# Kernel tuning notes

Measured on AMD Instinct MI355X. Metric: run time of the kernel, lower is better.

The kernel has to match this reference:

```python
import jax, jax.numpy as jnp
import numpy as np

N, NC, G, C = 80000, 8000, 16, 5
E, ES = 160000, 80000
NUM_OPS, OP_E, OP_F, CFG_F, H = 120, 32, 140, 18, 32
ALPHA = 0.2  # tf.nn.leaky_relu default slope

seg = jax.ops.segment_sum

def lrelu(x):
    return jnp.where(x >= 0, x, ALPHA * x)

def l2norm(x):
    s = jnp.sum(x * x, axis=-1, keepdims=True)
    return x * jax.lax.rsqrt(jnp.maximum(s, 1e-12))

def setup_inputs():
    k = jax.random.split(jax.random.key(0), 20)
    p = lambda i, shp, s=0.1: jax.random.normal(k[i], shp, jnp.float32) * s
    d_in = CFG_F + OP_F + OP_E  # 190: concat(config, op feats, op embed)
    d_gc = CFG_F + H            # 50: concat(config, hidden)
    return {
        'op_feats': jax.random.normal(k[0], (N, OP_F), jnp.float32),
        'config_feats': jax.random.normal(k[1], (NC, C, CFG_F), jnp.float32),
        'op_ids': jax.random.randint(k[2], (N,), 0, NUM_OPS),
        'selected': jax.random.randint(k[3], (N,), 0, 2) == 1,
        'feed_src': jax.random.randint(k[4], (E,), 0, N),
        'feed_dst': jax.random.randint(k[5], (E,), 0, N),
        'sfeed_src': jax.random.randint(k[6], (ES,), 0, N),
        'sfeed_dst': jax.random.randint(k[7], (ES,), 0, N),
        'config_src': jnp.arange(NC),
        'config_dst': jax.random.randint(k[8], (NC,), 0, N),
        'sconfig_src': jnp.arange(NC),
        'sconfig_dst': jax.random.randint(k[9], (NC,), 0, N),
        'op_gid': (jnp.arange(N) * G) // N,
        'cfg_gid': (jnp.arange(NC) * G) // NC,
        'emb': p(10, (NUM_OPS, OP_E), 1.0),
        'pre_w1': p(11, (d_in, H)), 'pre_b1': jnp.zeros((H,), jnp.float32),
        'pre_w2': p(12, (H, H)), 'pre_b2': jnp.zeros((H,), jnp.float32),
        'gc1_w1': p(13, (d_gc, H)), 'gc1_b1': jnp.zeros((H,), jnp.float32),
        'gc1_w2': p(14, (H, H)), 'gc1_b2': jnp.zeros((H,), jnp.float32),
        'gc2_w1': p(15, (d_gc, H)), 'gc2_b1': jnp.zeros((H,), jnp.float32),
        'gc2_w2': p(16, (H, H)), 'gc2_b2': jnp.zeros((H,), jnp.float32),
        'post_w1': p(17, (3 * H, H)),
        'post_w2': p(18, (H, 1)),
    }

def _mlp(x, w1, b1, w2, b2):
    return lrelu(x @ w1 + b1) @ w2 + b2

def _node_forward(nf, cf, src, dst, csrc, cdst, pre, gcs):
    # AdjacencyMultiplier('config') @ config_feats : scatter nconfig feats to ops
    cfg = 100.0 * seg(cf[csrc], cdst, num_segments=N)            # [N, C, 18]
    x = jnp.broadcast_to(nf[:, None, :], (N, C, nf.shape[-1]))   # stack over configs
    x = lrelu(_mlp(jnp.concatenate([cfg, x], -1), *pre))         # prenet + leaky_relu
    # A_hat = A + A^T + I with symmetric normalization D^-1/2 A_hat D^-1/2
    loop = jnp.arange(N)
    src_all = jnp.concatenate([src, dst, loop])
    dst_all = jnp.concatenate([dst, src, loop])
    inv = jax.lax.rsqrt(seg(jnp.ones(src_all.shape, nf.dtype), dst_all, num_segments=N))
    inv = inv[:, None, None]
    for gp in gcs:
        y = jnp.concatenate([cfg, x], -1) * inv
        y = seg(y[src_all], dst_all, num_segments=N) * inv       # A_hat_norm @ y
        x = x + lrelu(_mlp(y, *gp))                              # residual
    return x

def _forward(op_feats, config_feats, emb, pre, gc1, gc2, post_w1, post_w2,
             op_ids, selected, feed, sfeed, cfg_e, scfg_e, op_gid, cfg_gid):
    nf = jnp.concatenate([op_feats, emb[op_ids]], -1)            # [N, 172]
    x_full = _node_forward(jax.lax.stop_gradient(nf), jax.lax.stop_gradient(config_feats),
                           feed[0], feed[1], cfg_e[0], cfg_e[1], pre, (gc1, gc2))
    x_bp = _node_forward(nf, config_feats, sfeed[0], sfeed[1],
                         scfg_e[0], scfg_e[1], pre, (gc1, gc2))
    x = jnp.where(selected[:, None, None], x_bp, x_full)         # [N, C, H]
    cfg_nodes = seg(x[cfg_e[1]], cfg_e[0], num_segments=NC)      # adj_config^T @ x
    op_sum = seg(x, op_gid, num_segments=G)                      # [G, C, H]
    cnt = seg(jnp.ones((N,), x.dtype), op_gid, num_segments=G)
    op_mean = op_sum / cnt[:, None, None]
    cfg_sum = seg(cfg_nodes, cfg_gid, num_segments=G)
    feats = jnp.concatenate([op_mean, l2norm(op_sum), l2norm(cfg_sum)], -1)  # [G, C, 3H]
    return (lrelu(feats @ post_w1) @ post_w2)[..., 0]            # [G, C]

def reference(op_feats, config_feats, op_ids, selected, feed_src, feed_dst,
              sfeed_src, sfeed_dst, config_src, config_dst, sconfig_src, sconfig_dst,
              op_gid, cfg_gid, emb, pre_w1, pre_b1, pre_w2, pre_b2,
              gc1_w1, gc1_b1, gc1_w2, gc1_b2, gc2_w1, gc2_b1, gc2_w2, gc2_b2,
              post_w1, post_w2):
    return _forward(op_feats, config_feats, emb,
                    (pre_w1, pre_b1, pre_w2, pre_b2),
                    (gc1_w1, gc1_b1, gc1_w2, gc1_b2),
                    (gc2_w1, gc2_b1, gc2_w2, gc2_b2),
                    post_w1, post_w2,
                    op_ids, selected, (feed_src, feed_dst), (sfeed_src, sfeed_dst),
                    (config_src, config_dst), (sconfig_src, sconfig_dst), op_gid, cfg_gid)
```

## Files before the change

### kernel.cpp

```cpp
#include <hip/hip_runtime.h>
#include <hip/hip_bf16.h>
#include <math.h>

#define CDIV(a,b) (((a)+(b)-1)/(b))

constexpr int N_   = 80000;
constexpr int NC_  = 8000;
constexpr int G_   = 16;
constexpr int C_   = 5;
constexpr int CFGF = 18;
constexpr int OPF  = 140;
constexpr int OPE  = 32;
constexpr int H_   = 32;
constexpr int NUMOPS = 120;
constexpr int CROW = C_ * CFGF;
constexpr int XROW = C_ * H_;
constexpr float ALPHA_ = 0.2f;
constexpr int NPG = N_ / G_;
constexpr int EPG = NC_ / G_;

__device__ __forceinline__ float lrelu(float v) { return v >= 0.0f ? v : ALPHA_ * v; }

__global__ void k_nfwop(const float* __restrict__ emb, const float* __restrict__ w1,
                        const float* __restrict__ b1, float* __restrict__ nfwop) {
    int t = blockIdx.x * blockDim.x + threadIdx.x;
    if (t >= NUMOPS * H_) return;
    int op = t >> 5, h = t & 31;
    float a = b1[h];
    for (int e = 0; e < OPE; ++e)
        a = fmaf(emb[op * OPE + e], w1[(CFGF + OPF + e) * H_ + h], a);
    nfwop[t] = a;
}

__global__ void k_nfw(const float* __restrict__ opf, const int* __restrict__ op_ids,
                      const float* __restrict__ nfwop, const float* __restrict__ w1,
                      float* __restrict__ nfw) {
    int n = blockIdx.x * blockDim.x + threadIdx.x;
    if (n >= N_) return;
    float acc[H_];
    const float4* it = (const float4*)(nfwop + (size_t)op_ids[n] * H_);
    #pragma unroll
    for (int q = 0; q < 8; ++q) {
        float4 v = it[q];
        acc[4 * q + 0] = v.x; acc[4 * q + 1] = v.y; acc[4 * q + 2] = v.z; acc[4 * q + 3] = v.w;
    }
    const float4* f4 = (const float4*)(opf + (size_t)n * OPF);
    const float* wf = w1 + CFGF * H_;
    for (int kc = 0; kc < OPF / 4; ++kc) {
        float4 rv = f4[kc];
        float rs[4] = {rv.x, rv.y, rv.z, rv.w};
        #pragma unroll
        for (int j = 0; j < 4; ++j) {
            int k = kc * 4 + j;
            #pragma unroll
            for (int h = 0; h < H_; ++h) acc[h] = fmaf(rs[j], wf[k * H_ + h], acc[h]);
        }
    }
    float4* o = (float4*)(nfw + (size_t)n * H_);
    #pragma unroll
    for (int q = 0; q < 8; ++q)
        o[q] = make_float4(acc[4 * q], acc[4 * q + 1], acc[4 * q + 2], acc[4 * q + 3]);
}

__global__ void k_cfg_scatter(const float* __restrict__ cf, const int* __restrict__ cdst,
                              float* __restrict__ cfg) {
    int t = blockIdx.x * blockDim.x + threadIdx.x;
    if (t >= NC_ * CROW) return;
    int i = t / CROW, j = t - i * CROW;
    atomicAdd(&cfg[(size_t)cdst[i] * CROW + j], 100.0f * cf[t]);
}

__global__ void k_deg2(const int* __restrict__ s0, const int* __restrict__ d0, int E0,
                       const int* __restrict__ s1, const int* __restrict__ d1, int E1,
                       int* __restrict__ deg) {
    int e = blockIdx.x * blockDim.x + threadIdx.x;
    if (e < E0) {
        atomicAdd(&deg[s0[e]], 1);
        atomicAdd(&deg[d0[e]], 1);
    } else if (e < E0 + E1) {
        int e2 = e - E0;
        atomicAdd(&deg[N_ + s1[e2]], 1);
        atomicAdd(&deg[N_ + d1[e2]], 1);
    }
}

__global__ void k_inv2(const int* __restrict__ deg, float* __restrict__ inv) {
    int i = blockIdx.x * blockDim.x + threadIdx.x;
    if (i >= 2 * N_) return;
    inv[i] = 1.0f / sqrtf((float)(deg[i] + 1));
}

__global__ void k_scan1(const int* __restrict__ deg, int* __restrict__ roff, int* __restrict__ aux) {
    __shared__ int s[256];
    int t = threadIdx.x, n = blockIdx.x * 256 + t;
    int v = (n < 2 * N_) ? deg[n] : 0;
    s[t] = v; __syncthreads();
    for (int off = 1; off < 256; off <<= 1) {
        int x = (t >= off) ? s[t - off] : 0;
        __syncthreads();
        s[t] += x;
        __syncthreads();
    }
    if (n < 2 * N_) roff[n] = s[t] - v;
    if (t == 255) aux[blockIdx.x] = s[255];
}

__global__ void k_scan2(int* __restrict__ aux, int nb) {
    __shared__ int s[1024];
    int t = threadIdx.x;
    int v = (t < nb) ? aux[t] : 0;
    s[t] = v; __syncthreads();
    for (int off = 1; off < 1024; off <<= 1) {
        int x = (t >= off) ? s[t - off] : 0;
        __syncthreads();
        s[t] += x;
        __syncthreads();
    }
    if (t < nb) aux[t] = s[t] - v;
}

__global__ void k_scan3(int* __restrict__ roff, const int* __restrict__ aux,
                        int* __restrict__ cur, int total) {
    int n = blockIdx.x * blockDim.x + threadIdx.x;
    if (n < 2 * N_) {
        int r = roff[n] + aux[n >> 8];
        roff[n] = r;
        cur[n] = r;
    }
    if (n == 0) roff[2 * N_] = total;
}

__global__ void k_fill2(const int* __restrict__ s0, const int* __restrict__ d0, int E0,
                        const int* __restrict__ s1, const int* __restrict__ d1, int E1,
                        int* __restrict__ cur, int* __restrict__ col) {
    int e = blockIdx.x * blockDim.x + threadIdx.x;
    if (e < E0) {
        int s = s0[e], d = d0[e];
        col[atomicAdd(&cur[d], 1)] = s;
        col[atomicAdd(&cur[s], 1)] = d;
    } else if (e < E0 + E1) {
        int e2 = e - E0;
        int s = s1[e2], d = d1[e2];
        col[atomicAdd(&cur[N_ + d], 1)] = s;
        col[atomicAdd(&cur[N_ + s], 1)] = d;
    }
}

__global__ void k_csum_gather(const float2* __restrict__ cfg2, const float* __restrict__ inv,
                              const int* __restrict__ roff, const int* __restrict__ col,
                              float2* __restrict__ csum2) {
    int t = blockIdx.x * blockDim.x + threadIdx.x;
    if (t >= N_ * 45) return;
    int n = t / 45, j2 = t - n * 45;
    float iv = inv[n];
    float2 a = cfg2[t];
    a.x *= iv; a.y *= iv;
    int e = roff[n], p1 = roff[n + 1];
    for (; e + 1 < p1; e += 2) {
        int s0 = col[e], s1 = col[e + 1];
        float i0 = inv[s0], i1 = inv[s1];
        float2 v0 = cfg2[(size_t)s0 * 45 + j2];
        float2 v1 = cfg2[(size_t)s1 * 45 + j2];
        a.x = fmaf(v0.x, i0, a.x); a.y = fmaf(v0.y, i0, a.y);
        a.x = fmaf(v1.x, i1, a.x); a.y = fmaf(v1.y, i1, a.y);
    }
    if (e < p1) {
        int s0 = col[e];
        float i0 = inv[s0];
        float2 v0 = cfg2[(size_t)s0 * 45 + j2];
        a.x = fmaf(v0.x, i0, a.x); a.y = fmaf(v0.y, i0, a.y);
    }
    csum2[t] = a;
}

__global__ void k_pre(const float* __restrict__ cfg, const float* __restrict__ nfw,
                      const float* __restrict__ w1, const float* __restrict__ w2,
                      const float* __restrict__ b2, float* __restrict__ x) {
    int r = blockIdx.x * blockDim.x + threadIdx.x;
    if (r >= N_ * C_) return;
    int n = r / C_;
    float h1[H_];
    const float4* nf4 = (const float4*)(nfw + (size_t)n * H_);
    #pragma unroll
    for (int q = 0; q < 8; ++q) {
        float4 v = nf4[q];
        h1[4 * q + 0] = v.x; h1[4 * q + 1] = v.y; h1[4 * q + 2] = v.z; h1[4 * q + 3] = v.w;
    }
    const float2* c2 = (const float2*)(cfg + (size_t)r * CFGF);
    for (int kc = 0; kc < CFGF / 2; ++kc) {
        float2 cv = c2[kc];
        float cs[2] = {cv.x, cv.y};
        #pragma unroll
        for (int j = 0; j < 2; ++j) {
            int k = kc * 2 + j;
            #pragma unroll
            for (int h = 0; h < H_; ++h) h1[h] = fmaf(cs[j], w1[k * H_ + h], h1[h]);
        }
    }
    #pragma unroll
    for (int h = 0; h < H_; ++h) h1[h] = lrelu(h1[h]);
    float acc[H_];
    #pragma unroll
    for (int h = 0; h < H_; ++h) acc[h] = b2[h];
    #pragma unroll
    for (int k = 0; k < H_; ++k) {
        float v = h1[k];
        #pragma unroll
        for (int h = 0; h < H_; ++h) acc[h] = fmaf(v, w2[k * H_ + h], acc[h]);
    }
    float4* o = (float4*)(x + (size_t)r * H_);
    #pragma unroll
    for (int q = 0; q < 8; ++q)
        o[q] = make_float4(lrelu(acc[4 * q]), lrelu(acc[4 * q + 1]),
                           lrelu(acc[4 * q + 2]), lrelu(acc[4 * q + 3]));
}

__global__ void k_gcfused(const float4* __restrict__ xin4, const float* __restrict__ csum,
                          const float* __restrict__ inv, const int* __restrict__ roff,
                          const int* __restrict__ col,
                          const float* __restrict__ w1, const float* __restrict__ b1,
                          const float* __restrict__ w2, const float* __restrict__ b2,
                          float4* __restrict__ xout4) {
    int r = blockIdx.x * blockDim.x + threadIdx.x;
    if (r >= N_ * C_) return;
    int n = r / C_, c = r - n * C_;
    float iv = inv[n];
    float xs[H_];
    const float4* sp = xin4 + (size_t)r * 8;
    #pragma unroll
    for (int q = 0; q < 8; ++q) {
        float4 v = sp[q];
        xs[4 * q + 0] = v.x * iv; xs[4 * q + 1] = v.y * iv;
        xs[4 * q + 2] = v.z * iv; xs[4 * q + 3] = v.w * iv;
    }
    int e = roff[n], p1 = roff[n + 1];
    for (; e + 1 < p1; e += 2) {
        int s0 = col[e], s1 = col[e + 1];
        float i0 = inv[s0], i1 = inv[s1];
        const float4* np0 = xin4 + ((size_t)s0 * C_ + c) * 8;
        const float4* np1 = xin4 + ((size_t)s1 * C_ + c) * 8;
        #pragma unroll
        for (int q = 0; q < 8; ++q) {
            float4 v0 = np0[q];
            float4 v1 = np1[q];
            xs[4 * q + 0] = fmaf(v0.x, i0, xs[4 * q + 0]);
            xs[4 * q + 1] = fmaf(v0.y, i0, xs[4 * q + 1]);
            xs[4 * q + 2] = fmaf(v0.z, i0, xs[4 * q + 2]);
            xs[4 * q + 3] = fmaf(v0.w, i0, xs[4 * q + 3]);
            xs[4 * q + 0] = fmaf(v1.x, i1, xs[4 * q + 0]);
            xs[4 * q + 1] = fmaf(v1.y, i1, xs[4 * q + 1]);
            xs[4 * q + 2] = fmaf(v1.z, i1, xs[4 * q + 2]);
            xs[4 * q + 3] = fmaf(v1.w, i1, xs[4 * q + 3]);
        }
    }
    if (e < p1) {
        int s0 = col[e];
        float i0 = inv[s0];
        const float4* np = xin4 + ((size_t)s0 * C_ + c) * 8;
        #pragma unroll
        for (int q = 0; q < 8; ++q) {
            float4 v = np[q];
            xs[4 * q + 0] = fmaf(v.x, i0, xs[4 * q + 0]);
            xs[4 * q + 1] = fmaf(v.y, i0, xs[4 * q + 1]);
            xs[4 * q + 2] = fmaf(v.z, i0, xs[4 * q + 2]);
            xs[4 * q + 3] = fmaf(v.w, i0, xs[4 * q + 3]);
        }
    }
    float t1[H_];
    #pragma unroll
    for (int h = 0; h < H_; ++h) t1[h] = 0.0f;
    const float2* c2 = (const float2*)(csum + (size_t)r * CFGF);
    for (int kc = 0; kc < CFGF / 2; ++kc) {
        float2 cv = c2[kc];
        float cs[2] = {cv.x, cv.y};
        #pragma unroll
        for (int j = 0; j < 2; ++j) {
            int k = kc * 2 + j;
            #pragma unroll
            for (int h = 0; h < H_; ++h) t1[h] = fmaf(cs[j], w1[k * H_ + h], t1[h]);
        }
    }
    #pragma unroll
    for (int k = 0; k < H_; ++k) {
        float v = xs[k];
        #pragma unroll
        for (int h = 0; h < H_; ++h) t1[h] = fmaf(v, w1[(CFGF + k) * H_ + h], t1[h]);
    }
    float h1[H_];
    #pragma unroll
    for (int h = 0; h < H_; ++h) h1[h] = lrelu(fmaf(iv, t1[h], b1[h]));
    float acc[H_];
    #pragma unroll
    for (int h = 0; h < H_; ++h) acc[h] = b2[h];
    #pragma unroll
    for (int k = 0; k < H_; ++k) {
        float v = h1[k];
        #pragma unroll
        for (int h = 0; h < H_; ++h) acc[h] = fmaf(v, w2[k * H_ + h], acc[h]);
    }
    float4* o = xout4 + (size_t)r * 8;
    #pragma unroll
    for (int q = 0; q < 8; ++q) {
        float4 v = sp[q];
        v.x += lrelu(acc[4 * q + 0]); v.y += lrelu(acc[4 * q + 1]);
        v.z += lrelu(acc[4 * q + 2]); v.w += lrelu(acc[4 * q + 3]);
        o[q] = v;
    }
}

__global__ void k_opsum(const float4* __restrict__ xf4, const float4* __restrict__ xb4,
                        const int* __restrict__ sel,
                        float* __restrict__ osum, float* __restrict__ cnt) {
    __shared__ float4 ls[6 * G_ * 40];
    __shared__ float lc[6 * G_];
    for (int i = threadIdx.x; i < 6 * G_ * 40; i += blockDim.x) ls[i] = make_float4(0.f, 0.f, 0.f, 0.f);
    if (threadIdx.x < 6 * G_) lc[threadIdx.x] = 0.0f;
    __syncthreads();
    int j4 = threadIdx.x % 40, i = threadIdx.x / 40;
    const int NPB = CDIV(N_, 512);
    int start = blockIdx.x * NPB;
    int end = min(start + NPB, N_);
    if (i < 6) {
        for (int n = start + i; n < end; n += 6) {
            int g = n / NPG;
            const float4* xr = sel[n] ? xb4 : xf4;
            float4 v = xr[(size_t)n * 40 + j4];
            int o = (i * G_ + g) * 40 + j4;
            float4 cacc = ls[o];
            cacc.x += v.x; cacc.y += v.y; cacc.z += v.z; cacc.w += v.w;
            ls[o] = cacc;
            if (j4 == 0) lc[i * G_ + g] += 1.0f;
        }
    }
    __syncthreads();
    for (int idx = threadIdx.x; idx < G_ * 40; idx += blockDim.x) {
        float4 s = ls[idx];
        #pragma unroll
        for (int q = 1; q < 6; ++q) {
            float4 v = ls[q * G_ * 40 + idx];
            s.x += v.x; s.y += v.y; s.z += v.z; s.w += v.w;
        }
        int g = idx / 40, j = idx - g * 40;
        float* o = osum + (size_t)g * XROW + j * 4;
        atomicAdd(o + 0, s.x); atomicAdd(o + 1, s.y);
        atomicAdd(o + 2, s.z); atomicAdd(o + 3, s.w);
    }
    if (threadIdx.x < G_) {
        float c = 0.0f;
        #pragma unroll
        for (int q = 0; q < 6; ++q) c += lc[q * G_ + threadIdx.x];
        atomicAdd(&cnt[threadIdx.x], c);
    }
}

__global__ void k_cfgsum(const float4* __restrict__ xf4, const float4* __restrict__ xb4,
                         const int* __restrict__ sel, const int* __restrict__ cdst,
                         float* __restrict__ gsum) {
    __shared__ float4 ls[6 * G_ * 40];
    for (int i = threadIdx.x; i < 6 * G_ * 40; i += blockDim.x) ls[i] = make_float4(0.f, 0.f, 0.f, 0.f);
    __syncthreads();
    int j4 = threadIdx.x % 40, i = threadIdx.x / 40;
    const int EPB = CDIV(NC_, 64);
    int start = blockIdx.x * EPB;
    int end = min(start + EPB, NC_);
    if (i < 6) {
        for (int e = start + i; e < end; e += 6) {
            int g = e / EPG;
            int n = cdst[e];
            const float4* xr = sel[n] ? xb4 : xf4;
            float4 v = xr[(size_t)n * 40 + j4];
            int o = (i * G_ + g) * 40 + j4;
            float4 cacc = ls[o];
            cacc.x += v.x; cacc.y += v.y; cacc.z += v.z; cacc.w += v.w;
            ls[o] = cacc;
        }
    }
    __syncthreads();
    for (int idx = threadIdx.x; idx < G_ * 40; idx += blockDim.x) {
        float4 s = ls[idx];
        #pragma unroll
        for (int q = 1; q < 6; ++q) {
            float4 v = ls[q * G_ * 40 + idx];
            s.x += v.x; s.y += v.y; s.z += v.z; s.w += v.w;
        }
        int g = idx / 40, j = idx - g * 40;
        float* o = gsum + (size_t)g * XROW + j * 4;
        atomicAdd(o + 0, s.x); atomicAdd(o + 1, s.y);
        atomicAdd(o + 2, s.z); atomicAdd(o + 3, s.w);
    }
}

__global__ void k_final(const float* __restrict__ osum, const float* __restrict__ gsum,
                        const float* __restrict__ cnt, const float* __restrict__ pw1,
                        const float* __restrict__ pw2, float* __restrict__ out) {
    __shared__ float sw1[3 * H_ * H_];
    __shared__ float sw2[H_];
    for (int i = threadIdx.x; i < 3 * H_ * H_; i += blockDim.x) sw1[i] = pw1[i];
    if (threadIdx.x < H_) sw2[threadIdx.x] = pw2[threadIdx.x];
    __syncthreads();
    int t = threadIdx.x;
    if (t >= G_ * C_) return;
    int g = t / C_;
    const float* os = osum + (size_t)t * H_;
    const float* cs = gsum + (size_t)t * H_;
    float icnt = 1.0f / cnt[g];
    float a0[H_], a1[H_], a2[H_];
    float s1 = 0.0f, s2 = 0.0f;
    #pragma unroll
    for (int h = 0; h < H_; ++h) {
        float v1 = os[h], v2 = cs[h];
        a0[h] = v1 * icnt;
        a1[h] = v1; s1 = fmaf(v1, v1, s1);
        a2[h] = v2; s2 = fmaf(v2, v2, s2);
    }
    float r1 = 1.0f / sqrtf(fmaxf(s1, 1e-12f));
    float r2 = 1.0f / sqrtf(fmaxf(s2, 1e-12f));
    #pragma unroll
    for (int h = 0; h < H_; ++h) { a1[h] *= r1; a2[h] *= r2; }
    float o = 0.0f;
    #pragma unroll
    for (int h = 0; h < H_; ++h) {
        float a = 0.0f;
        #pragma unroll
        for (int k = 0; k < H_; ++k) a = fmaf(a0[k], sw1[k * H_ + h], a);
        #pragma unroll
        for (int k = 0; k < H_; ++k) a = fmaf(a1[k], sw1[(H_ + k) * H_ + h], a);
        #pragma unroll
        for (int k = 0; k < H_; ++k) a = fmaf(a2[k], sw1[(2 * H_ + k) * H_ + h], a);
        o = fmaf(lrelu(a), sw2[h], o);
    }
    out[t] = o;
}

extern "C" void kernel_launch(void* const* d_in, const int* in_sizes, int n_in,
                              void* d_out, int out_size, void* d_ws, size_t ws_size,
                              hipStream_t stream) {
    const float* op_feats     = (const float*)d_in[0];
    const float* config_feats = (const float*)d_in[1];
    const int*   op_ids       = (const int*)d_in[2];
    const int*   selected     = (const int*)d_in[3];
    const int*   feed_src     = (const int*)d_in[4];
    const int*   feed_dst     = (const int*)d_in[5];
    const int*   sfeed_src    = (const int*)d_in[6];
    const int*   sfeed_dst    = (const int*)d_in[7];
    const int*   config_dst   = (const int*)d_in[9];
    const int*   sconfig_dst  = (const int*)d_in[11];
    const float* emb          = (const float*)d_in[14];
    const float* pre_w1       = (const float*)d_in[15];
    const float* pre_b1       = (const float*)d_in[16];
    const float* pre_w2       = (const float*)d_in[17];
    const float* pre_b2       = (const float*)d_in[18];
    const float* gc_w1[2]     = {(const float*)d_in[19], (const float*)d_in[23]};
    const float* gc_b1[2]     = {(const float*)d_in[20], (const float*)d_in[24]};
    const float* gc_w2[2]     = {(const float*)d_in[21], (const float*)d_in[25]};
    const float* gc_b2[2]     = {(const float*)d_in[22], (const float*)d_in[26]};
    const float* post_w1      = (const float*)d_in[27];
    const float* post_w2      = (const float*)d_in[28];

    int E0 = in_sizes[4], E1 = in_sizes[6];

    char* ws = (char*)d_ws;
    size_t off = 0;
    auto alloc = [&](size_t bytes) { void* p = ws + off; off += (bytes + 255) & ~(size_t)255; return p; };
    float* nfw   = (float*)alloc((size_t)N_ * H_ * 4);
    float* nfwop = (float*)alloc((size_t)NUMOPS * H_ * 4);
    float* cfg   = (float*)alloc((size_t)N_ * CROW * 4);
    float* csum  = (float*)alloc((size_t)N_ * CROW * 4);
    float* xf    = (float*)alloc((size_t)N_ * XROW * 4);
    float* xb    = (float*)alloc((size_t)N_ * XROW * 4);
    float* xscr  = (float*)alloc((size_t)N_ * XROW * 4);
    float* invA  = (float*)alloc((size_t)2 * N_ * 4);
    int*   degA  = (int*)alloc((size_t)2 * N_ * 4);
    int*   roffA = (int*)alloc((size_t)(2 * N_ + 1) * 4);
    int*   curA  = (int*)alloc((size_t)2 * N_ * 4);
    int*   aux   = (int*)alloc((size_t)1024 * 4);
    int*   colA  = (int*)alloc((size_t)2 * (E0 + E1) * 4);
    float* osum  = (float*)alloc((size_t)G_ * XROW * 4);
    float* gsum  = (float*)alloc((size_t)G_ * XROW * 4);
    float* cntb  = (float*)alloc((size_t)G_ * 4);

    const int NB1 = CDIV(2 * N_, 256);

    k_nfwop<<<CDIV(NUMOPS * H_, 256), 256, 0, stream>>>(emb, pre_w1, pre_b1, nfwop);
    k_nfw<<<CDIV(N_, 256), 256, 0, stream>>>(op_feats, op_ids, nfwop, pre_w1, nfw);

    hipMemsetAsync(degA, 0, (size_t)2 * N_ * 4, stream);
    k_deg2<<<CDIV(E0 + E1, 256), 256, 0, stream>>>(feed_src, feed_dst, E0,
                                                   sfeed_src, sfeed_dst, E1, degA);
    k_inv2<<<CDIV(2 * N_, 256), 256, 0, stream>>>(degA, invA);
    k_scan1<<<NB1, 256, 0, stream>>>(degA, roffA, aux);
    k_scan2<<<1, 1024, 0, stream>>>(aux, NB1);
    k_scan3<<<CDIV(2 * N_, 256), 256, 0, stream>>>(roffA, aux, curA, 2 * (E0 + E1));
    k_fill2<<<CDIV(E0 + E1, 256), 256, 0, stream>>>(feed_src, feed_dst, E0,
                                                    sfeed_src, sfeed_dst, E1, curA, colA);

    for (int p = 0; p < 2; ++p) {
        const int* cdst = p ? sconfig_dst : config_dst;
        float* x0 = p ? xb : xf;
        const float* ivp = invA + (size_t)p * N_;
        const int* roffp = roffA + (size_t)p * N_;

        hipMemsetAsync(cfg, 0, (size_t)N_ * CROW * 4, stream);
        k_cfg_scatter<<<CDIV(NC_ * CROW, 256), 256, 0, stream>>>(config_feats, cdst, cfg);
        k_csum_gather<<<CDIV(N_ * 45, 256), 256, 0, stream>>>((const float2*)cfg, ivp, roffp,
                                                              colA, (float2*)csum);
        k_pre<<<CDIV(N_ * C_, 256), 256, 0, stream>>>(cfg, nfw, pre_w1, pre_w2, pre_b2, x0);

        k_gcfused<<<CDIV(N_ * C_, 256), 256, 0, stream>>>((const float4*)x0, csum, ivp, roffp,
                                                          colA, gc_w1[0], gc_b1[0], gc_w2[0],
                                                          gc_b2[0], (float4*)xscr);
        k_gcfused<<<CDIV(N_ * C_, 256), 256, 0, stream>>>((const float4*)xscr, csum, ivp, roffp,
                                                          colA, gc_w1[1], gc_b1[1], gc_w2[1],
                                                          gc_b2[1], (float4*)x0);
    }

    hipMemsetAsync(osum, 0, (size_t)(2 * G_ * XROW + G_) * 4, stream);
    k_opsum<<<512, 256, 0, stream>>>((const float4*)xf, (const float4*)xb, selected, osum, cntb);
    k_cfgsum<<<64, 256, 0, stream>>>((const float4*)xf, (const float4*)xb, selected,
                                     config_dst, gsum);
    k_final<<<1, 128, 0, stream>>>(osum, gsum, cntb, post_w1, post_w2, (float*)d_out);
}
```

Measured before the change: 715.9 us.

## Sort nodes by degree so gather wavefronts process similar neighbor counts

Adds a per-graph degree histogram, a bucket scan and a counting sort that build a node permutation ordered by descending degree. The neighbor-gather kernels for config sums and graph convolution now map each thread to a permuted node. Threads in a wavefront therefore iterate over similar neighbor counts, which is meant to cut divergence and idle lanes in the edge loops. In exchange it adds three small launches plus atomics, and reads and writes of each node's own row no longer follow thread order, which may hurt coalescing.

```diff
diff --git a/kernel.cpp b/kernel.cpp
--- a/kernel.cpp
+++ b/kernel.cpp
@@ -146,16 +146,45 @@
     }
 }
 
+__global__ void k_hist(const int* __restrict__ deg, int* __restrict__ hist) {
+    int i = blockIdx.x * blockDim.x + threadIdx.x;
+    if (i >= 2 * N_) return;
+    int b = (i >= N_ ? 256 : 0) + min(deg[i], 255);
+    atomicAdd(&hist[b], 1);
+}
+
+__global__ void k_hscan(const int* __restrict__ hist, int* __restrict__ cur) {
+    __shared__ int s[512];
+    int t = threadIdx.x;
+    s[t] = hist[t];
+    __syncthreads();
+    int half = t & 256, d = t & 255;
+    int sum = 0;
+    for (int dd = d + 1; dd < 256; ++dd) sum += s[half + dd];
+    cur[t] = sum;
+}
+
+__global__ void k_psort(const int* __restrict__ deg, int* __restrict__ cur,
+                        int* __restrict__ perm) {
+    int i = blockIdx.x * blockDim.x + threadIdx.x;
+    if (i >= 2 * N_) return;
+    int p = i >= N_;
+    int b = (p ? 256 : 0) + min(deg[i], 255);
+    int pos = atomicAdd(&cur[b], 1);
+    perm[p * N_ + pos] = i - p * N_;
+}
+
 __global__ void k_csum_gather(const float2* __restrict__ cfg2, const float* __restrict__ inv,
                               const int* __restrict__ roff, const int* __restrict__ col,
-                              float2* __restrict__ csum2) {
+                              const int* __restrict__ perm, float2* __restrict__ csum2) {
     int t = blockIdx.x * blockDim.x + threadIdx.x;
     if (t >= N_ * 45) return;
-    int n = t / 45, j2 = t - n * 45;
-    float iv = inv[n];
-    float2 a = cfg2[t];
+    int q = t / 45, j2 = t - q * 45;
+    int nl = perm[q];
+    float iv = inv[nl];
+    float2 a = cfg2[(size_t)nl * 45 + j2];
     a.x *= iv; a.y *= iv;
-    int e = roff[n], p1 = roff[n + 1];
+    int e = roff[nl], p1 = roff[nl + 1];
     for (; e + 1 < p1; e += 2) {
         int s0 = col[e], s1 = col[e + 1];
         float i0 = inv[s0], i1 = inv[s1];
@@ -217,40 +246,41 @@
 
 __global__ void k_gcfused(const float4* __restrict__ xin4, const float* __restrict__ csum,
                           const float* __restrict__ inv, const int* __restrict__ roff,
-                          const int* __restrict__ col,
+                          const int* __restrict__ col, const int* __restrict__ perm,
                           const float* __restrict__ w1, const float* __restrict__ b1,
                           const float* __restrict__ w2, const float* __restrict__ b2,
                           float4* __restrict__ xout4) {
     int r = blockIdx.x * blockDim.x + threadIdx.x;
     if (r >= N_ * C_) return;
-    int n = r / C_, c = r - n * C_;
-    float iv = inv[n];
+    int q = r / C_, c = r - q * C_;
+    int nl = perm[q];
+    float iv = inv[nl];
     float xs[H_];
-    const float4* sp = xin4 + (size_t)r * 8;
-    #pragma unroll
-    for (int q = 0; q < 8; ++q) {
-        float4 v = sp[q];
-        xs[4 * q + 0] = v.x * iv; xs[4 * q + 1] = v.y * iv;
-        xs[4 * q + 2] = v.z * iv; xs[4 * q + 3] = v.w * iv;
-    }
-    int e = roff[n], p1 = roff[n + 1];
+    const float4* sp = xin4 + ((size_t)nl * C_ + c) * 8;
+    #pragma unroll
+    for (int qq = 0; qq < 8; ++qq) {
+        float4 v = sp[qq];
+        xs[4 * qq + 0] = v.x * iv; xs[4 * qq + 1] = v.y * iv;
+        xs[4 * qq + 2] = v.z * iv; xs[4 * qq + 3] = v.w * iv;
+    }
+    int e = roff[nl], p1 = roff[nl + 1];
     for (; e + 1 < p1; e += 2) {
         int s0 = col[e], s1 = col[e + 1];
         float i0 = inv[s0], i1 = inv[s1];
         const float4* np0 = xin4 + ((size_t)s0 * C_ + c) * 8;
         const float4* np1 = xin4 + ((size_t)s1 * C_ + c) * 8;
         #pragma unroll
-        for (int q = 0; q < 8; ++q) {
-            float4 v0 = np0[q];
-            float4 v1 = np1[q];
-            xs[4 * q + 0] = fmaf(v0.x, i0, xs[4 * q + 0]);
-            xs[4 * q + 1] = fmaf(v0.y, i0, xs[4 * q + 1]);
-            xs[4 * q + 2] = fmaf(v0.z, i0, xs[4 * q + 2]);
-            xs[4 * q + 3] = fmaf(v0.w, i0, xs[4 * q + 3]);
-            xs[4 * q + 0] = fmaf(v1.x, i1, xs[4 * q + 0]);
-            xs[4 * q + 1] = fmaf(v1.y, i1, xs[4 * q + 1]);
-            xs[4 * q + 2] = fmaf(v1.z, i1, xs[4 * q + 2]);
-            xs[4 * q + 3] = fmaf(v1.w, i1, xs[4 * q + 3]);
+        for (int qq = 0; qq < 8; ++qq) {
+            float4 v0 = np0[qq];
+            float4 v1 = np1[qq];
+            xs[4 * qq + 0] = fmaf(v0.x, i0, xs[4 * qq + 0]);
+            xs[4 * qq + 1] = fmaf(v0.y, i0, xs[4 * qq + 1]);
+            xs[4 * qq + 2] = fmaf(v0.z, i0, xs[4 * qq + 2]);
+            xs[4 * qq + 3] = fmaf(v0.w, i0, xs[4 * qq + 3]);
+            xs[4 * qq + 0] = fmaf(v1.x, i1, xs[4 * qq + 0]);
+            xs[4 * qq + 1] = fmaf(v1.y, i1, xs[4 * qq + 1]);
+            xs[4 * qq + 2] = fmaf(v1.z, i1, xs[4 * qq + 2]);
+            xs[4 * qq + 3] = fmaf(v1.w, i1, xs[4 * qq + 3]);
         }
     }
     if (e < p1) {
@@ -258,12 +288,12 @@
         float i0 = inv[s0];
         const float4* np = xin4 + ((size_t)s0 * C_ + c) * 8;
         #pragma unroll
-        for (int q = 0; q < 8; ++q) {
-            float4 v = np[q];
-            xs[4 * q + 0] = fmaf(v.x, i0, xs[4 * q + 0]);
-            xs[4 * q + 1] = fmaf(v.y, i0, xs[4 * q + 1]);
-            xs[4 * q + 2] = fmaf(v.z, i0, xs[4 * q + 2]);
-            xs[4 * q + 3] = fmaf(v.w, i0, xs[4 * q + 3]);
+        for (int qq = 0; qq < 8; ++qq) {
+            float4 v = np[qq];
+            xs[4 * qq + 0] = fmaf(v.x, i0, xs[4 * qq + 0]);
+            xs[4 * qq + 1] = fmaf(v.y, i0, xs[4 * qq + 1]);
+            xs[4 * qq + 2] = fmaf(v.z, i0, xs[4 * qq + 2]);
+            xs[4 * qq + 3] = fmaf(v.w, i0, xs[4 * qq + 3]);
         }
     }
     float t1[H_];
@@ -298,13 +328,13 @@
         #pragma unroll
         for (int h = 0; h < H_; ++h) acc[h] = fmaf(v, w2[k * H_ + h], acc[h]);
     }
-    float4* o = xout4 + (size_t)r * 8;
-    #pragma unroll
-    for (int q = 0; q < 8; ++q) {
-        float4 v = sp[q];
-        v.x += lrelu(acc[4 * q + 0]); v.y += lrelu(acc[4 * q + 1]);
-        v.z += lrelu(acc[4 * q + 2]); v.w += lrelu(acc[4 * q + 3]);
-        o[q] = v;
+    float4* o = xout4 + ((size_t)nl * C_ + c) * 8;
+    #pragma unroll
+    for (int qq = 0; qq < 8; ++qq) {
+        float4 v = sp[qq];
+        v.x += lrelu(acc[4 * qq + 0]); v.y += lrelu(acc[4 * qq + 1]);
+        v.z += lrelu(acc[4 * qq + 2]); v.w += lrelu(acc[4 * qq + 3]);
+        o[qq] = v;
     }
 }
 
@@ -475,6 +505,9 @@
     int*   curA  = (int*)alloc((size_t)2 * N_ * 4);
     int*   aux   = (int*)alloc((size_t)1024 * 4);
     int*   colA  = (int*)alloc((size_t)2 * (E0 + E1) * 4);
+    int*   permA = (int*)alloc((size_t)2 * N_ * 4);
+    int*   hist  = (int*)alloc((size_t)512 * 4);
+    int*   hcur  = (int*)alloc((size_t)512 * 4);
     float* osum  = (float*)alloc((size_t)G_ * XROW * 4);
     float* gsum  = (float*)alloc((size_t)G_ * XROW * 4);
     float* cntb  = (float*)alloc((size_t)G_ * 4);
@@ -485,6 +518,7 @@
     k_nfw<<<CDIV(N_, 256), 256, 0, stream>>>(op_feats, op_ids, nfwop, pre_w1, nfw);
 
     hipMemsetAsync(degA, 0, (size_t)2 * N_ * 4, stream);
+    hipMemsetAsync(hist, 0, (size_t)512 * 4, stream);
     k_deg2<<<CDIV(E0 + E1, 256), 256, 0, stream>>>(feed_src, feed_dst, E0,
                                                    sfeed_src, sfeed_dst, E1, degA);
     k_inv2<<<CDIV(2 * N_, 256), 256, 0, stream>>>(degA, invA);
@@ -493,25 +527,29 @@
     k_scan3<<<CDIV(2 * N_, 256), 256, 0, stream>>>(roffA, aux, curA, 2 * (E0 + E1));
     k_fill2<<<CDIV(E0 + E1, 256), 256, 0, stream>>>(feed_src, feed_dst, E0,
                                                     sfeed_src, sfeed_dst, E1, curA, colA);
+    k_hist<<<CDIV(2 * N_, 256), 256, 0, stream>>>(degA, hist);
+    k_hscan<<<1, 512, 0, stream>>>(hist, hcur);
+    k_psort<<<CDIV(2 * N_, 256), 256, 0, stream>>>(degA, hcur, permA);
 
     for (int p = 0; p < 2; ++p) {
         const int* cdst = p ? sconfig_dst : config_dst;
         float* x0 = p ? xb : xf;
         const float* ivp = invA + (size_t)p * N_;
         const int* roffp = roffA + (size_t)p * N_;
+        const int* permp = permA + (size_t)p * N_;
 
         hipMemsetAsync(cfg, 0, (size_t)N_ * CROW * 4, stream);
         k_cfg_scatter<<<CDIV(NC_ * CROW, 256), 256, 0, stream>>>(config_feats, cdst, cfg);
         k_csum_gather<<<CDIV(N_ * 45, 256), 256, 0, stream>>>((const float2*)cfg, ivp, roffp,
-                                                              colA, (float2*)csum);
+                                                              colA, permp, (float2*)csum);
         k_pre<<<CDIV(N_ * C_, 256), 256, 0, stream>>>(cfg, nfw, pre_w1, pre_w2, pre_b2, x0);
 
         k_gcfused<<<CDIV(N_ * C_, 256), 256, 0, stream>>>((const float4*)x0, csum, ivp, roffp,
-                                                          colA, gc_w1[0], gc_b1[0], gc_w2[0],
-                                                          gc_b2[0], (float4*)xscr);
+                                                          colA, permp, gc_w1[0], gc_b1[0],
+                                                          gc_w2[0], gc_b2[0], (float4*)xscr);
         k_gcfused<<<CDIV(N_ * C_, 256), 256, 0, stream>>>((const float4*)xscr, csum, ivp, roffp,
-                                                          colA, gc_w1[1], gc_b1[1], gc_w2[1],
-                                                          gc_b2[1], (float4*)x0);
+                                                          colA, permp, gc_w1[1], gc_b1[1],
+                                                          gc_w2[1], gc_b2[1], (float4*)x0);
     }
 
     hipMemsetAsync(osum, 0, (size_t)(2 * G_ * XROW + G_) * 4, stream);
```

Result: slower. 1.688 ms (+135.8%).
